# Kernel tuning notes

Hardware: AMD Instinct MI355X
Metric: run time of the kernel (lower is better)

## Reference

```python
import jax, jax.numpy as jnp
import numpy as np

N_HEADS = 32
N_KV_HEADS = 8
HEAD_DIM = 64  # dim // n_heads = 2048 // 32
ROPE_BASE = 10000.0


def rotate_half(x):
    x1, x2 = jnp.split(x, 2, axis=-1)
    return jnp.concatenate((-x2, x1), axis=-1)


def setup_inputs() -> dict:
    key = jax.random.key(0)
    ks = jax.random.split(key, 6)
    b, s, d = 2, 2048, 2048
    kv_d = N_KV_HEADS * HEAD_DIM  # 512
    x = jax.random.normal(ks[0], (b, s, d), dtype=jnp.float32)
    mask = jnp.zeros((1, 1, s, s), dtype=jnp.float32)  # additive attn mask
    position_ids = jnp.tile(jnp.arange(s, dtype=jnp.int32)[None, :], (b, 1))
    scale = 0.02
    wq = jax.random.normal(ks[1], (d, d), dtype=jnp.float32) * scale
    wk = jax.random.normal(ks[2], (kv_d, d), dtype=jnp.float32) * scale
    wv = jax.random.normal(ks[3], (kv_d, d), dtype=jnp.float32) * scale
    wo = jax.random.normal(ks[4], (d, d), dtype=jnp.float32) * scale
    return {"x": x, "mask": mask, "position_ids": position_ids,
            "wq": wq, "wk": wk, "wv": wv, "wo": wo}


def reference(x, mask, position_ids, wq, wk, wv, wo):
    b, s, d = x.shape
    n_rep = N_HEADS // N_KV_HEADS

    # Fused-style QKV projections (torch Linear: y = x @ W^T)
    xq = jnp.einsum('bsd,fd->bsf', x, wq).reshape(b, s, N_HEADS, HEAD_DIM)
    xk = jnp.einsum('bsd,fd->bsf', x, wk).reshape(b, s, N_KV_HEADS, HEAD_DIM)
    xv = jnp.einsum('bsd,fd->bsf', x, wv).reshape(b, s, N_KV_HEADS, HEAD_DIM)

    # RoPE cache
    inv_freq = 1.0 / (ROPE_BASE ** (jnp.arange(0, HEAD_DIM, 2, dtype=jnp.float32) / HEAD_DIM))
    t = jnp.arange(s, dtype=jnp.float32)
    freqs = t[:, None] * inv_freq[None, :]            # [s, hd/2]
    emb = jnp.concatenate((freqs, freqs), axis=-1)    # [s, hd]
    cos = jnp.cos(emb)[position_ids][:, :, None, :]   # [b, s, 1, hd]
    sin = jnp.sin(emb)[position_ids][:, :, None, :]

    xq = xq * cos + rotate_half(xq) * sin
    xk = xk * cos + rotate_half(xk) * sin

    # Grouped-query attention without materializing repeated K/V:
    # q: [b, g, r, s, hd] where g=n_kv_heads, r=n_rep; k,v: [b, g, s, hd]
    q = xq.reshape(b, s, N_KV_HEADS, n_rep, HEAD_DIM).transpose(0, 2, 3, 1, 4)
    k = xk.transpose(0, 2, 1, 3)
    v = xv.transpose(0, 2, 1, 3)

    scale = 1.0 / jnp.sqrt(jnp.asarray(HEAD_DIM, dtype=x.dtype))
    scores = jnp.einsum('bgrqd,bgkd->bgrqk', q, k) * scale
    scores = scores + mask[:, :, None, :, :]          # broadcast over (g, r)
    attn = jax.nn.softmax(scores, axis=-1)
    out = jnp.einsum('bgrqk,bgkd->bgrqd', attn, v)    # [b, g, r, s, hd]
    out = out.transpose(0, 3, 1, 2, 4).reshape(b, s, N_HEADS * HEAD_DIM)
    return jnp.einsum('bsf,df->bsd', out, wo)
```

## Files before the change

kernel.cpp:

```cpp
#include <hip/hip_runtime.h>
#include <hip/hip_bf16.h>


typedef __attribute__((ext_vector_type(8))) short bf16x8;
typedef __attribute__((ext_vector_type(4))) float f32x4;

static __device__ __forceinline__ unsigned short f2bf(float f) {
  union { float f; unsigned u; } v; v.f = f;
  unsigned r = v.u + 0x7FFFu + ((v.u >> 16) & 1u);
  return (unsigned short)(r >> 16);
}
static __device__ __forceinline__ float bf2f(unsigned short h) {
  union { unsigned u; float f; } v; v.u = ((unsigned)h) << 16;
  return v.f;
}
static __device__ __forceinline__ unsigned pk_bf2(float lo, float hi) {
  union { __hip_bfloat162 h; unsigned u; } v;
  v.h = __float22bfloat162_rn(float2{lo, hi});
  return v.u;
}
static __device__ __forceinline__ float exp2_fast(float x) {
  float r;
  asm("v_exp_f32 %0, %1" : "=v"(r) : "v"(x));
  return r;
}
static __device__ __forceinline__ void gload16(const unsigned short* g, unsigned short* l) {
  __builtin_amdgcn_global_load_lds((const __attribute__((address_space(1))) unsigned*)g,
                                   (__attribute__((address_space(3))) unsigned*)l,
                                   16, 0, 0);
}

__global__ __launch_bounds__(256) void cvt_all(const float* __restrict__ x,
                                               const float* __restrict__ wq,
                                               const float* __restrict__ wk,
                                               const float* __restrict__ wv,
                                               const float* __restrict__ wo,
                                               unsigned short* __restrict__ xb,
                                               unsigned short* __restrict__ wqb,
                                               unsigned short* __restrict__ wkb,
                                               unsigned short* __restrict__ wvb,
                                               unsigned short* __restrict__ wob) {
  int bid = (int)blockIdx.x;
  const float* s; unsigned short* d; int rel;
  if      (bid < 4096) { s = x;  d = xb;  rel = bid; }
  else if (bid < 6144) { s = wq; d = wqb; rel = bid - 4096; }
  else if (bid < 6656) { s = wk; d = wkb; rel = bid - 6144; }
  else if (bid < 7168) { s = wv; d = wvb; rel = bid - 6656; }
  else                 { s = wo; d = wob; rel = bid - 7168; }
  size_t i = (size_t)rel * 256 + threadIdx.x;
  const float4* sp = reinterpret_cast<const float4*>(s) + i * 2;
  float4 a = sp[0], b = sp[1];
  bf16x8 o;
  o[0] = (short)f2bf(a.x); o[1] = (short)f2bf(a.y);
  o[2] = (short)f2bf(a.z); o[3] = (short)f2bf(a.w);
  o[4] = (short)f2bf(b.x); o[5] = (short)f2bf(b.y);
  o[6] = (short)f2bf(b.z); o[7] = (short)f2bf(b.w);
  reinterpret_cast<bf16x8*>(d)[i] = o;
}

__global__ __launch_bounds__(256) void rope_table(float2* __restrict__ tab) {
  int i = (int)blockIdx.x * 256 + threadIdx.x;
  int s = i >> 5, d = i & 31;
  float ang = (float)s * __expf(-(float)d * 0.28782313662425572f);
  float sv, cv;
  sincosf(ang, &sv, &cv);
  tab[i] = float2{cv, sv};
}

template<int MODE>
__global__ __launch_bounds__(512, 2) void gemm256(const unsigned short* __restrict__ A,
                                                  const unsigned short* __restrict__ B0,
                                                  const unsigned short* __restrict__ B1,
                                                  const unsigned short* __restrict__ B2,
                                                  void* __restrict__ C0,
                                                  void* __restrict__ C1,
                                                  void* __restrict__ C2,
                                                  const int* __restrict__ pos,
                                                  const float2* __restrict__ tab) {
  __shared__ __align__(16) unsigned short lA[2][2][256 * 32];
  __shared__ __align__(16) unsigned short lB[2][2][256 * 32];
  const int tid  = threadIdx.x;
  const int lane = tid & 63, w = tid >> 6;
  const int l15  = lane & 15, l4 = lane >> 4;
  const int wr   = w >> 2, wc = w & 3;

  const int NB  = (MODE == 0) ? 12 : 8;
  const int CPX = (MODE == 0) ? 24 : 16;
  int bid = (int)blockIdx.x;
  bid = (bid & 7) * CPX + (bid >> 3);
  const int bm = bid / NB, bn = bid % NB;
  const int brow = bm << 8;

  const unsigned short* Bp; int bcolB;
  if (MODE == 1)    { Bp = B0; bcolB = bn << 8; }
  else if (bn < 8)  { Bp = B0; bcolB = bn << 8; }
  else if (bn < 10) { Bp = B1; bcolB = (bn - 8) << 8; }
  else              { Bp = B2; bcolB = (bn - 10) << 8; }

  auto stageh = [&](int t, int buf, int h) {
    const int kk = h >> 1;
    const unsigned short* src = (h & 1) ? Bp : A;
    const int rbase = (h & 1) ? bcolB : brow;
    unsigned short* dst = (h & 1) ? lB[buf][kk] : lA[buf][kk];
    #pragma unroll
    for (int i = 0; i < 2; ++i) {
      int row = (i << 7) + (tid >> 2);
      int cg  = (tid & 3) ^ ((row >> 1) & 3);
      int lb  = ((i << 9) + (w << 6)) << 3;
      gload16(src + (size_t)(rbase + row) * 2048 + (t << 6) + (kk << 5) + (cg << 3),
              dst + lb);
    }
  };

  f32x4 acc[8][4] = {};

  stageh(0, 0, 0); stageh(0, 0, 1); stageh(0, 0, 2); stageh(0, 0, 3);

  for (int t = 0; t < 32; ++t) {
    const int buf = t & 1;
    #pragma unroll
    for (int kk = 0; kk < 2; ++kk) {
      if (t < 31) asm volatile("s_waitcnt vmcnt(4)" ::: "memory");
      else        asm volatile("s_waitcnt vmcnt(0)" ::: "memory");
      asm volatile("s_barrier" ::: "memory");

      bf16x8 bfr[4], af0[4], af1[4];
      #pragma unroll
      for (int nt = 0; nt < 4; ++nt) {
        int rb = wc * 64 + nt * 16 + l15;
        bfr[nt] = *(const bf16x8*)(lB[buf][kk] + rb * 32 + ((l4 ^ ((rb >> 1) & 3)) << 3));
      }
      #pragma unroll
      for (int mt = 0; mt < 4; ++mt) {
        int ra0 = wr * 128 + mt * 16 + l15;
        af0[mt] = *(const bf16x8*)(lA[buf][kk] + ra0 * 32 + ((l4 ^ ((ra0 >> 1) & 3)) << 3));
        int ra1 = wr * 128 + 64 + mt * 16 + l15;
        af1[mt] = *(const bf16x8*)(lA[buf][kk] + ra1 * 32 + ((l4 ^ ((ra1 >> 1) & 3)) << 3));
      }
      if (t < 31) { stageh(t + 1, buf ^ 1, kk << 1); stageh(t + 1, buf ^ 1, (kk << 1) | 1); }

      __builtin_amdgcn_s_setprio(1);
      #pragma unroll
      for (int mt = 0; mt < 4; ++mt)
        #pragma unroll
        for (int nt = 0; nt < 4; ++nt)
          acc[mt][nt] = __builtin_amdgcn_mfma_f32_16x16x32_bf16(
              af0[mt], bfr[nt], acc[mt][nt], 0, 0, 0);
      #pragma unroll
      for (int mt = 0; mt < 4; ++mt)
        #pragma unroll
        for (int nt = 0; nt < 4; ++nt)
          acc[4 + mt][nt] = __builtin_amdgcn_mfma_f32_16x16x32_bf16(
              af1[mt], bfr[nt], acc[4 + mt][nt], 0, 0, 0);
      __builtin_amdgcn_s_setprio(0);
    }
  }

  if (MODE == 0 && bn < 10) {
    const float scl = (bn < 8) ? 0.18033688013509544f : 1.0f;
    #pragma unroll
    for (int mf = 0; mf < 8; ++mf)
      #pragma unroll
      for (int r = 0; r < 4; ++r) {
        int m = brow + wr * 128 + mf * 16 + l4 * 4 + r;
        int p = pos[m];
        float2 t0 = tab[p * 32 + l15];
        float2 t1 = tab[p * 32 + 16 + l15];
        float c0 = t0.x * scl, s0 = t0.y * scl;
        float c1 = t1.x * scl, s1 = t1.y * scl;
        float lo0 = acc[mf][0][r], hi0 = acc[mf][2][r];
        acc[mf][0][r] = lo0 * c0 - hi0 * s0;
        acc[mf][2][r] = hi0 * c0 + lo0 * s0;
        float lo1 = acc[mf][1][r], hi1 = acc[mf][3][r];
        acc[mf][1][r] = lo1 * c1 - hi1 * s1;
        acc[mf][3][r] = hi1 * c1 + lo1 * s1;
      }
  }

  #pragma unroll
  for (int mf = 0; mf < 8; ++mf)
    #pragma unroll
    for (int nf = 0; nf < 4; ++nf)
      #pragma unroll
      for (int r = 0; r < 4; ++r) {
        int m  = brow + wr * 128 + mf * 16 + l4 * 4 + r;
        int nl = bcolB + wc * 64 + nf * 16 + l15;
        float v = acc[mf][nf][r];
        if (MODE == 1) {
          ((float*)C0)[(size_t)m * 2048 + nl] = v;
        } else if (bn < 8) {
          ((unsigned short*)C0)[(size_t)m * 2048 + nl] = f2bf(v);
        } else if (bn < 10) {
          ((unsigned short*)C1)[(size_t)m * 512 + nl] = f2bf(v);
        } else {
          int b = m >> 11, s = m & 2047;
          ((unsigned short*)C2)[((size_t)b * 512 + nl) * 2048 + s] = f2bf(v);
        }
      }
}

__global__ __launch_bounds__(256, 4) void flash_attn(const unsigned short* __restrict__ Q,
                                                     const unsigned short* __restrict__ Kq,
                                                     const unsigned short* __restrict__ Vt,
                                                     unsigned short* __restrict__ AO) {
  int bid = (int)blockIdx.x;
  bid = (bid & 7) * 128 + (bid >> 3);
  const int qb = bid & 15, bh = bid >> 4;
  const int b = bh >> 5, h = bh & 31, g = h >> 2;
  const int tid = threadIdx.x;
  const int lane = tid & 63, w = tid >> 6;
  const int l15 = lane & 15, l4 = lane >> 4;

  __shared__ __align__(16) unsigned short klds[2][64 * 72];
  __shared__ __align__(16) unsigned short vlds[2][64 * 72];

  const int qw = qb * 128 + w * 32;
  bf16x8 qa[2][2];
  #pragma unroll
  for (int qt = 0; qt < 2; ++qt) {
    const unsigned short* qbase = Q + (((size_t)b * 2048 + qw + qt * 16 + l15) * 32 + h) * 64;
    qa[qt][0] = *(const bf16x8*)(qbase + l4 * 8);
    qa[qt][1] = *(const bf16x8*)(qbase + 32 + l4 * 8);
  }

  const int srow0 = tid >> 3, srow1 = srow0 + 32, scol = (tid & 7) << 3;
  const unsigned short* Kbase = Kq + (size_t)b * 1048576 + (size_t)g * 64;
  const unsigned short* Vbase = Vt + ((size_t)b * 8 + g) * 131072;

  f32x4 acc_o[2][4] = {};
  float rsum[2] = {0.f, 0.f};
  bf16x8 kreg0, kreg1, vreg0, vreg1;

  kreg0 = *(const bf16x8*)(Kbase + (size_t)srow0 * 512 + scol);
  kreg1 = *(const bf16x8*)(Kbase + (size_t)srow1 * 512 + scol);
  vreg0 = *(const bf16x8*)(Vbase + (size_t)srow0 * 2048 + scol);
  vreg1 = *(const bf16x8*)(Vbase + (size_t)srow1 * 2048 + scol);
  *(bf16x8*)(klds[0] + srow0 * 72 + scol) = kreg0;
  *(bf16x8*)(klds[0] + srow1 * 72 + scol) = kreg1;
  *(bf16x8*)(vlds[0] + srow0 * 72 + scol) = vreg0;
  *(bf16x8*)(vlds[0] + srow1 * 72 + scol) = vreg1;
  __syncthreads();

  int cur = 0;

  for (int kb = 0; kb < 32; ++kb) {
    if (kb != 31) {
      int kn = (kb + 1) * 64;
      kreg0 = *(const bf16x8*)(Kbase + (size_t)(kn + srow0) * 512 + scol);
      kreg1 = *(const bf16x8*)(Kbase + (size_t)(kn + srow1) * 512 + scol);
      vreg0 = *(const bf16x8*)(Vbase + (size_t)srow0 * 2048 + kn + scol);
      vreg1 = *(const bf16x8*)(Vbase + (size_t)srow1 * 2048 + kn + scol);
    }

    const unsigned short* kl = klds[cur];
    f32x4 sT[2][4];
    __builtin_amdgcn_s_setprio(1);
    #pragma unroll
    for (int mt = 0; mt < 4; ++mt) {
      int rk = mt * 16 + l15;
      bf16x8 af0 = *(const bf16x8*)(kl + rk * 72 + l4 * 8);
      bf16x8 af1 = *(const bf16x8*)(kl + rk * 72 + 32 + l4 * 8);
      #pragma unroll
      for (int qt = 0; qt < 2; ++qt) {
        f32x4 z = {};
        z = __builtin_amdgcn_mfma_f32_16x16x32_bf16(af0, qa[qt][0], z, 0, 0, 0);
        sT[qt][mt] = __builtin_amdgcn_mfma_f32_16x16x32_bf16(af1, qa[qt][1], z, 0, 0, 0);
      }
    }
    __builtin_amdgcn_s_setprio(0);

    unsigned pkx[2][4], pky[2][4];
    #pragma unroll
    for (int qt = 0; qt < 2; ++qt)
      #pragma unroll
      for (int mt = 0; mt < 4; ++mt) {
        float p0 = exp2_fast(sT[qt][mt][0]), p1 = exp2_fast(sT[qt][mt][1]);
        float p2 = exp2_fast(sT[qt][mt][2]), p3 = exp2_fast(sT[qt][mt][3]);
        rsum[qt] += (p0 + p1) + (p2 + p3);
        pkx[qt][mt] = pk_bf2(p0, p1);
        pky[qt][mt] = pk_bf2(p2, p3);
      }

    const unsigned short* vl = vlds[cur];
    #pragma unroll
    for (int kt = 0; kt < 2; ++kt) {
      bf16x8 vf[4];
      #pragma unroll
      for (int mt = 0; mt < 4; ++mt) {
        int rd = mt * 16 + l15;
        union { struct { uint2 a, b; } p; bf16x8 v; } vu;
        vu.p.a = *(const uint2*)(vl + rd * 72 + kt * 32 + l4 * 4);
        vu.p.b = *(const uint2*)(vl + rd * 72 + kt * 32 + 16 + l4 * 4);
        vf[mt] = vu.v;
      }
      __builtin_amdgcn_s_setprio(1);
      #pragma unroll
      for (int qt = 0; qt < 2; ++qt) {
        union { uint4 u; bf16x8 v; } pu;
        pu.u = uint4{pkx[qt][2 * kt], pky[qt][2 * kt],
                     pkx[qt][2 * kt + 1], pky[qt][2 * kt + 1]};
        #pragma unroll
        for (int mt = 0; mt < 4; ++mt)
          acc_o[qt][mt] = __builtin_amdgcn_mfma_f32_16x16x32_bf16(vf[mt], pu.v,
                                                                  acc_o[qt][mt], 0, 0, 0);
      }
      __builtin_amdgcn_s_setprio(0);
    }

    if (kb != 31) {
      unsigned short* kd = klds[cur ^ 1];
      unsigned short* vd = vlds[cur ^ 1];
      *(bf16x8*)(kd + srow0 * 72 + scol) = kreg0;
      *(bf16x8*)(kd + srow1 * 72 + scol) = kreg1;
      *(bf16x8*)(vd + srow0 * 72 + scol) = vreg0;
      *(bf16x8*)(vd + srow1 * 72 + scol) = vreg1;
    }
    __syncthreads();
    cur ^= 1;
  }

  #pragma unroll
  for (int qt = 0; qt < 2; ++qt) {
    float rs = rsum[qt];
    rs += __shfl_xor(rs, 16, 64);
    rs += __shfl_xor(rs, 32, 64);
    float inv = 1.0f / rs;
    unsigned short* obase = AO + (((size_t)b * 2048 + qw + qt * 16 + l15) * 32 + h) * 64;
    #pragma unroll
    for (int mt = 0; mt < 4; ++mt) {
      uint2 w2;
      w2.x = pk_bf2(acc_o[qt][mt][0] * inv, acc_o[qt][mt][1] * inv);
      w2.y = pk_bf2(acc_o[qt][mt][2] * inv, acc_o[qt][mt][3] * inv);
      *(uint2*)(obase + mt * 16 + l4 * 4) = w2;
    }
  }
}

extern "C" void kernel_launch(void* const* d_in, const int* in_sizes, int n_in,
                              void* d_out, int out_size, void* d_ws, size_t ws_size,
                              hipStream_t stream) {
  const float* x  = (const float*)d_in[0];
  const int*   pos = (const int*)d_in[2];
  const float* wq = (const float*)d_in[3];
  const float* wk = (const float*)d_in[4];
  const float* wv = (const float*)d_in[5];
  const float* wo = (const float*)d_in[6];

  size_t off = 0;
  char* ws = (char*)d_ws;
  auto nxt = [&](size_t bytes) { char* p = ws + off; off += bytes; return (unsigned short*)p; };
  const size_t NEED = 79691776ull;
  bool small_ws = ws_size < NEED;
  unsigned short* xb  = small_ws ? (unsigned short*)d_out : nxt(16777216);
  unsigned short* wqb = nxt(8388608);
  unsigned short* wkb = nxt(2097152);
  unsigned short* wvb = nxt(2097152);
  unsigned short* wob = nxt(8388608);
  unsigned short* Qb  = nxt(16777216);
  unsigned short* Kb  = nxt(4194304);
  unsigned short* Vtb = nxt(4194304);
  unsigned short* AOb = nxt(16777216);

  float2* tab = (float2*)AOb;

  cvt_all<<<9216, 256, 0, stream>>>(x, wq, wk, wv, wo, xb, wqb, wkb, wvb, wob);

  rope_table<<<256, 256, 0, stream>>>(tab);

  gemm256<0><<<192, 512, 0, stream>>>(xb, wqb, wkb, wvb, Qb, Kb, Vtb, pos, tab);

  flash_attn<<<1024, 256, 0, stream>>>(Qb, Kb, Vtb, AOb);

  gemm256<1><<<128, 512, 0, stream>>>(AOb, wob, nullptr, nullptr, d_out, nullptr, nullptr,
                                      nullptr, nullptr);
}
```

Baseline: 249.4 us.

## Stage K/V tiles with direct global-to-LDS loads and XOR-swizzled layout

Replaces the register-staged K/V copy (global load into VGPRs, then an LDS store after compute) with direct global-to-LDS loads (gload16) issued at the top of each iteration into the other buffer. The padded 72-element rows become an unpadded 32-column half-split layout with an XOR swizzle to avoid bank conflicts, and both the K and V fragment reads are rewritten to match. This is meant to free VGPRs and remove the LDS write pass. In exchange, the loop now waits for vmcnt(0) and a barrier at the start of every iteration, which may expose load latency.

Result: faster. 237.2 us (-4.9%).

```diff
diff --git a/kernel.cpp b/kernel.cpp
--- a/kernel.cpp
+++ b/kernel.cpp
@@ -211,8 +211,8 @@
   const int lane = tid & 63, w = tid >> 6;
   const int l15 = lane & 15, l4 = lane >> 4;
 
-  __shared__ __align__(16) unsigned short klds[2][64 * 72];
-  __shared__ __align__(16) unsigned short vlds[2][64 * 72];
+  __shared__ __align__(16) unsigned short klds[2][2 * 64 * 32];
+  __shared__ __align__(16) unsigned short vlds[2][2 * 64 * 32];
 
   const int qw = qb * 128 + w * 32;
   bf16x8 qa[2][2];
@@ -223,34 +223,33 @@
     qa[qt][1] = *(const bf16x8*)(qbase + 32 + l4 * 8);
   }
 
-  const int srow0 = tid >> 3, srow1 = srow0 + 32, scol = (tid & 7) << 3;
   const unsigned short* Kbase = Kq + (size_t)b * 1048576 + (size_t)g * 64;
   const unsigned short* Vbase = Vt + ((size_t)b * 8 + g) * 131072;
 
+  auto stage = [&](int kb, int buf) {
+    #pragma unroll
+    for (int i = 0; i < 2; ++i) {
+      int c   = (i << 8) + tid;
+      int sub = (c >> 2) & 63, half = c >> 8;
+      int scc = (c & 3) ^ ((sub >> 1) & 3);
+      int dst = c << 3;
+      gload16(Kbase + (size_t)(kb * 64 + sub) * 512 + (half << 5) + (scc << 3),
+              klds[buf] + dst);
+      gload16(Vbase + (size_t)sub * 2048 + kb * 64 + (half << 5) + (scc << 3),
+              vlds[buf] + dst);
+    }
+  };
+
   f32x4 acc_o[2][4] = {};
   float rsum[2] = {0.f, 0.f};
-  bf16x8 kreg0, kreg1, vreg0, vreg1;
-
-  kreg0 = *(const bf16x8*)(Kbase + (size_t)srow0 * 512 + scol);
-  kreg1 = *(const bf16x8*)(Kbase + (size_t)srow1 * 512 + scol);
-  vreg0 = *(const bf16x8*)(Vbase + (size_t)srow0 * 2048 + scol);
-  vreg1 = *(const bf16x8*)(Vbase + (size_t)srow1 * 2048 + scol);
-  *(bf16x8*)(klds[0] + srow0 * 72 + scol) = kreg0;
-  *(bf16x8*)(klds[0] + srow1 * 72 + scol) = kreg1;
-  *(bf16x8*)(vlds[0] + srow0 * 72 + scol) = vreg0;
-  *(bf16x8*)(vlds[0] + srow1 * 72 + scol) = vreg1;
-  __syncthreads();
-
+
+  stage(0, 0);
   int cur = 0;
 
   for (int kb = 0; kb < 32; ++kb) {
-    if (kb != 31) {
-      int kn = (kb + 1) * 64;
-      kreg0 = *(const bf16x8*)(Kbase + (size_t)(kn + srow0) * 512 + scol);
-      kreg1 = *(const bf16x8*)(Kbase + (size_t)(kn + srow1) * 512 + scol);
-      vreg0 = *(const bf16x8*)(Vbase + (size_t)srow0 * 2048 + kn + scol);
-      vreg1 = *(const bf16x8*)(Vbase + (size_t)srow1 * 2048 + kn + scol);
-    }
+    asm volatile("s_waitcnt vmcnt(0)" ::: "memory");
+    asm volatile("s_barrier" ::: "memory");
+    if (kb != 31) stage(kb + 1, cur ^ 1);
 
     const unsigned short* kl = klds[cur];
     f32x4 sT[2][4];
@@ -258,8 +257,9 @@
     #pragma unroll
     for (int mt = 0; mt < 4; ++mt) {
       int rk = mt * 16 + l15;
-      bf16x8 af0 = *(const bf16x8*)(kl + rk * 72 + l4 * 8);
-      bf16x8 af1 = *(const bf16x8*)(kl + rk * 72 + 32 + l4 * 8);
+      int sw = (l4 ^ ((rk >> 1) & 3)) << 3;
+      bf16x8 af0 = *(const bf16x8*)(kl + rk * 32 + sw);
+      bf16x8 af1 = *(const bf16x8*)(kl + 2048 + rk * 32 + sw);
       #pragma unroll
       for (int qt = 0; qt < 2; ++qt) {
         f32x4 z = {};
@@ -288,9 +288,11 @@
       #pragma unroll
       for (int mt = 0; mt < 4; ++mt) {
         int rd = mt * 16 + l15;
+        int s_ = (rd >> 1) & 3;
+        const unsigned short* vrow = vl + kt * 2048 + rd * 32 + ((l4 & 1) << 2);
         union { struct { uint2 a, b; } p; bf16x8 v; } vu;
-        vu.p.a = *(const uint2*)(vl + rd * 72 + kt * 32 + l4 * 4);
-        vu.p.b = *(const uint2*)(vl + rd * 72 + kt * 32 + 16 + l4 * 4);
+        vu.p.a = *(const uint2*)(vrow + ((((l4 >> 1))     ^ s_) << 3));
+        vu.p.b = *(const uint2*)(vrow + ((((l4 >> 1) | 2) ^ s_) << 3));
         vf[mt] = vu.v;
       }
       __builtin_amdgcn_s_setprio(1);
@@ -307,15 +309,6 @@
       __builtin_amdgcn_s_setprio(0);
     }
 
-    if (kb != 31) {
-      unsigned short* kd = klds[cur ^ 1];
-      unsigned short* vd = vlds[cur ^ 1];
-      *(bf16x8*)(kd + srow0 * 72 + scol) = kreg0;
-      *(bf16x8*)(kd + srow1 * 72 + scol) = kreg1;
-      *(bf16x8*)(vd + srow0 * 72 + scol) = vreg0;
-      *(bf16x8*)(vd + srow1 * 72 + scol) = vreg1;
-    }
-    __syncthreads();
     cur ^= 1;
   }
 
```
